# Kernel optimization log

Hardware: AMD Instinct MI355X
Metric: run time of the kernel (lower is better)

## Reference

```python
import jax, jax.numpy as jnp
import numpy as np
import math

B, T, D, H = 4, 1024, 1024, 16
DK = D // H
EPS = 1e-12  # F.normalize eps

def setup_inputs() -> dict:
    key = jax.random.key(0)
    ks = jax.random.split(key, 6)
    xav = math.sqrt(6.0 / (D + D))  # xavier_uniform bound for square Linear
    x = jax.random.normal(ks[0], (B, T, D), dtype=jnp.float32)
    Wq = jax.random.uniform(ks[1], (D, D), jnp.float32, -xav, xav)
    Wk = jax.random.uniform(ks[2], (D, D), jnp.float32, -xav, xav)
    Wv = jax.random.uniform(ks[3], (D, D), jnp.float32, -xav, xav)
    Wo = jax.random.uniform(ks[4], (D, D), jnp.float32, -xav, xav)
    logit_g = math.log(0.9 / 0.1)
    logit_l = math.log(0.1 / 0.9)
    W_gamma = jnp.zeros((H,), jnp.float32)
    b_gamma = jnp.full((H,), logit_g, jnp.float32)
    W_lambda = jnp.zeros((H,), jnp.float32)
    b_lambda = jnp.full((H,), logit_l, jnp.float32)
    return {"x": x, "Wq": Wq, "Wk": Wk, "Wv": Wv, "Wo": Wo,
            "W_gamma": W_gamma, "b_gamma": b_gamma,
            "W_lambda": W_lambda, "b_lambda": b_lambda}

def reference(x, Wq, Wk, Wv, Wo, W_gamma, b_gamma, W_lambda, b_lambda):
    b, t, d = x.shape
    # projections (torch Linear: x @ W.T), split heads -> [T, B, H, dk] for scan
    def proj(W):
        return jnp.einsum('btd,ed->bte', x, W).reshape(b, t, H, DK).transpose(1, 0, 2, 3)
    q = proj(Wq)
    k = proj(Wk)
    v = proj(Wv)
    # L2-normalize k along dk (F.normalize semantics)
    k = k / jnp.maximum(jnp.linalg.norm(k, axis=-1, keepdims=True), EPS)
    k_bar = k.mean(axis=-1)  # [T, B, H]
    gamma = jax.nn.sigmoid(W_gamma * k_bar + b_gamma)
    lam = jax.nn.sigmoid(W_lambda * k_bar + b_lambda)
    rho = (1.0 - lam) * gamma  # [T, B, H]

    S0 = jnp.zeros((b, H, DK, DK), x.dtype)

    def step(S, inp):
        q_t, k_t, v_t, rho_t = inp  # [B,H,dk] x3, [B,H]
        r = rho_t[..., None, None]
        S = r * S + (1.0 - r) * jnp.einsum('bhv,bhk->bhvk', v_t, k_t)
        y_t = jnp.einsum('bhv,bhvk->bhk', q_t, S)
        return S, y_t

    _, ys = jax.lax.scan(step, S0, (q, k, v, rho))  # ys: [T, B, H, dk]
    out = ys.transpose(1, 0, 2, 3).reshape(b, t, d)
    return jnp.einsum('btd,ed->bte', out, Wo)
```

## Files before the change

### kernel.cpp

```cpp
#include <hip/hip_runtime.h>
#include <hip/hip_bf16.h>


typedef __bf16 b16x8 __attribute__((ext_vector_type(8)));
typedef float  f32x4 __attribute__((ext_vector_type(4)));
typedef unsigned short u16x8 __attribute__((ext_vector_type(8)));
using bf16_t = __hip_bfloat16;

#define AS1C(p) ((const __attribute__((address_space(1))) void*)(p))
#define AS3(p)  ((__attribute__((address_space(3))) void*)(p))

__device__ __forceinline__ void g2l16(const void* g, void* l) {
  __builtin_amdgcn_global_load_lds(AS1C(g), AS3(l), 16, 0, 0);
}
__device__ __forceinline__ void g2l4(const void* g, void* l) {
  __builtin_amdgcn_global_load_lds(AS1C(g), AS3(l), 4, 0, 0);
}

__device__ __forceinline__ unsigned short f2b(float x) {
  unsigned u = __float_as_uint(x);
  return (unsigned short)((u + 0x7FFFu + ((u >> 16) & 1u)) >> 16);
}
__device__ __forceinline__ float b2f(unsigned short b) {
  return __uint_as_float(((unsigned)b) << 16);
}

__device__ __forceinline__ int wire_flag(const unsigned* __restrict__ x, int tid) {
  unsigned u = x[tid & 63];
  int e = (int)((u >> 23) & 0xFF);
  unsigned long long m = __ballot(e >= 95 && e <= 135);
  return (__popcll(m) >= 32) ? 1 : 0;
}

__global__ __launch_bounds__(256)
void convert_all(const void* __restrict__ x,
                 const void* __restrict__ w0, const void* __restrict__ w1,
                 const void* __restrict__ w2, const void* __restrict__ w3,
                 unsigned short* __restrict__ xb,
                 unsigned short* __restrict__ wb0, unsigned short* __restrict__ wb1,
                 unsigned short* __restrict__ wb2, unsigned short* __restrict__ wb3)
{
  const int fm = wire_flag((const unsigned*)x, threadIdx.x);
  const long i8 = ((long)blockIdx.x * 256 + threadIdx.x) * 8;
  const void* src; unsigned short* dst; long off;
  if (i8 < 4194304) { src = x; dst = xb; off = i8; }
  else {
    long j = i8 - 4194304;
    int w = (int)(j >> 20); off = j & 1048575;
    src = (w == 0) ? w0 : (w == 1) ? w1 : (w == 2) ? w2 : w3;
    dst = (w == 0) ? wb0 : (w == 1) ? wb1 : (w == 2) ? wb2 : wb3;
  }
  if (fm) {
    const float4 a = *(const float4*)((const float*)src + off);
    const float4 b = *(const float4*)((const float*)src + off + 4);
    u16x8 o;
    o[0] = f2b(a.x); o[1] = f2b(a.y); o[2] = f2b(a.z); o[3] = f2b(a.w);
    o[4] = f2b(b.x); o[5] = f2b(b.y); o[6] = f2b(b.z); o[7] = f2b(b.w);
    *(u16x8*)(dst + off) = o;
  } else {
    *(int4*)(dst + off) = *(const int4*)((const unsigned short*)src + off);
  }
}

__global__ __launch_bounds__(256)
void gemm_qkv(const unsigned* __restrict__ xraw,
              const bf16_t* __restrict__ A,
              const bf16_t* __restrict__ B0, const bf16_t* __restrict__ B1,
              const bf16_t* __restrict__ B2,
              unsigned short* __restrict__ C0, unsigned short* __restrict__ C1,
              unsigned short* __restrict__ C2,
              const void* __restrict__ Wg, const void* __restrict__ bg,
              const void* __restrict__ Wl, const void* __restrict__ bl,
              float* __restrict__ rho)
{
  constexpr int K = 1024, N = 1024;
  const int z = blockIdx.z;
  const bf16_t* B = (z == 0) ? B0 : (z == 1) ? B1 : B2;
  unsigned short* C = (z == 0) ? C0 : (z == 1) ? C1 : C2;
  __shared__ __align__(16) unsigned short As[128 * 32];
  __shared__ __align__(16) unsigned short Bs[128 * 32];
  const int tid  = threadIdx.x;
  const int lane = tid & 63;
  const int wave = tid >> 6;
  const int wm = wave >> 1, wn = wave & 1;
  const int quad = lane >> 4, tm = lane & 15;
  const long row0 = (long)blockIdx.y * 128;
  const long col0 = (long)blockIdx.x * 128;

  f32x4 acc[4][4];
#pragma unroll
  for (int i = 0; i < 4; ++i)
#pragma unroll
    for (int j = 0; j < 4; ++j) acc[i][j] = (f32x4){0.f, 0.f, 0.f, 0.f};

  const int sr = tid >> 2;
  const int scc = tid & 3;
  const int qg = (scc - (sr >> 1)) & 3;
  const bf16_t* ap = A + (row0 + sr) * (long)K + qg * 8;
  const bf16_t* bp = B + (col0 + sr) * (long)K + qg * 8;
  unsigned short* la = As + tid * 8;
  unsigned short* lb = Bs + tid * 8;
  const int cc = (quad + ((tm >> 1) & 3)) & 3;

  for (int kt = 0; kt < K; kt += 32) {
    __syncthreads();
    g2l16(ap + kt,           la);
    g2l16(ap + 64l * K + kt, la + 2048);
    g2l16(bp + kt,           lb);
    g2l16(bp + 64l * K + kt, lb + 2048);
    __syncthreads();

    b16x8 af[4], bfr[4];
#pragma unroll
    for (int i = 0; i < 4; ++i)
      af[i] = *(const b16x8*)&As[(wm * 64 + i * 16 + tm) * 32 + cc * 8];
#pragma unroll
    for (int j = 0; j < 4; ++j)
      bfr[j] = *(const b16x8*)&Bs[(wn * 64 + j * 16 + tm) * 32 + cc * 8];
#pragma unroll
    for (int i = 0; i < 4; ++i)
#pragma unroll
      for (int j = 0; j < 4; ++j)
        acc[i][j] = __builtin_amdgcn_mfma_f32_16x16x32_bf16(af[i], bfr[j], acc[i][j], 0, 0, 0);
  }

  if (z != 1) {
#pragma unroll
    for (int i = 0; i < 4; ++i)
#pragma unroll
      for (int j = 0; j < 4; ++j)
#pragma unroll
        for (int r = 0; r < 4; ++r) {
          long row = row0 + wm * 64 + i * 16 + quad * 4 + r;
          long col = col0 + wn * 64 + j * 16 + tm;
          C[row * N + col] = f2b(acc[i][j][r]);
        }
  } else {
    const int fm = wire_flag(xraw, tid);
    const int h = blockIdx.x * 2 + wn;
    float wgv, bgv, wlv, blv;
    if (fm) {
      wgv = ((const float*)Wg)[h]; bgv = ((const float*)bg)[h];
      wlv = ((const float*)Wl)[h]; blv = ((const float*)bl)[h];
    } else {
      wgv = b2f(((const unsigned short*)Wg)[h]); bgv = b2f(((const unsigned short*)bg)[h]);
      wlv = b2f(((const unsigned short*)Wl)[h]); blv = b2f(((const unsigned short*)bl)[h]);
    }
#pragma unroll
    for (int i = 0; i < 4; ++i)
#pragma unroll
      for (int r = 0; r < 4; ++r) {
        float ss = 0.f, sv = 0.f;
#pragma unroll
        for (int j = 0; j < 4; ++j) {
          const float v = acc[i][j][r];
          ss += v * v; sv += v;
        }
#pragma unroll
        for (int m = 1; m < 16; m <<= 1) {
          ss += __shfl_xor(ss, m);
          sv += __shfl_xor(sv, m);
        }
        const float inv = 1.f / fmaxf(sqrtf(ss), 1e-12f);
        const long row = row0 + wm * 64 + i * 16 + quad * 4 + r;
#pragma unroll
        for (int j = 0; j < 4; ++j)
          C[row * N + col0 + wn * 64 + j * 16 + tm] = f2b(acc[i][j][r] * inv);
        if (tm == 0) {
          const float kbar = sv * inv * (1.f / 64.f);
          const float gm = 1.f / (1.f + expf(-(wgv * kbar + bgv)));
          const float lm = 1.f / (1.f + expf(-(wlv * kbar + blv)));
          const int b = (int)(row >> 10), t = (int)(row & 1023);
          rho[(size_t)(b * 16 + h) * 1024 + t] = (1.f - lm) * gm;
        }
      }
  }
}

__global__ __launch_bounds__(256)
void gemm_out64(const unsigned* __restrict__ xraw,
                const bf16_t* __restrict__ A, const bf16_t* __restrict__ B,
                void* __restrict__ C)
{
  constexpr int K = 1024, N = 1024;
  __shared__ __align__(16) unsigned short As[64 * 64];
  __shared__ __align__(16) unsigned short Bs[64 * 64];
  const int tid  = threadIdx.x;
  const int lane = tid & 63;
  const int wave = tid >> 6;
  const int quad = lane >> 4, tm = lane & 15;
  const long row0 = (long)blockIdx.y * 64;
  const long col0 = (long)blockIdx.x * 64;

  f32x4 acc[4];
#pragma unroll
  for (int i = 0; i < 4; ++i) acc[i] = (f32x4){0.f, 0.f, 0.f, 0.f};

  const int sr = tid >> 2;
  const int scc = tid & 3;
  const int qg = (scc - (sr >> 1)) & 3;
  const bf16_t* ap = A + (row0 + sr) * (long)K + qg * 8;
  const bf16_t* bp = B + (col0 + sr) * (long)K + qg * 8;
  unsigned short* la = As + tid * 8;
  unsigned short* lb = Bs + tid * 8;
  const int cc = (quad + ((tm >> 1) & 3)) & 3;

  for (int kt = 0; kt < K; kt += 64) {
    __syncthreads();
    g2l16(ap + kt,      la);
    g2l16(ap + kt + 32, la + 2048);
    g2l16(bp + kt,      lb);
    g2l16(bp + kt + 32, lb + 2048);
    __syncthreads();

    b16x8 bf0 = *(const b16x8*)&Bs[(wave * 16 + tm) * 32 + cc * 8];
    b16x8 bf1 = *(const b16x8*)&Bs[2048 + (wave * 16 + tm) * 32 + cc * 8];
#pragma unroll
    for (int i = 0; i < 4; ++i) {
      b16x8 a0 = *(const b16x8*)&As[(i * 16 + tm) * 32 + cc * 8];
      b16x8 a1 = *(const b16x8*)&As[2048 + (i * 16 + tm) * 32 + cc * 8];
      acc[i] = __builtin_amdgcn_mfma_f32_16x16x32_bf16(a0, bf0, acc[i], 0, 0, 0);
      acc[i] = __builtin_amdgcn_mfma_f32_16x16x32_bf16(a1, bf1, acc[i], 0, 0, 0);
    }
  }

  const int fm = wire_flag(xraw, tid);
#pragma unroll
  for (int i = 0; i < 4; ++i)
#pragma unroll
    for (int r = 0; r < 4; ++r) {
      const long row = row0 + i * 16 + quad * 4 + r;
      const long col = col0 + wave * 16 + tm;
      const float v = acc[i][r];
      if (fm) ((float*)C)[row * N + col] = v;
      else    ((unsigned short*)C)[row * N + col] = f2b(v);
    }
}

__device__ __forceinline__ void stage_chunk(const unsigned short* G, int n0c, int h,
                                            unsigned short* lds, int tid) {
#pragma unroll
  for (int sh = 0; sh < 2; ++sh) {
    const int idx = sh * 256 + tid;
    const int row = idx >> 3, col = (idx & 7) * 8;
    g2l16(G + (size_t)(n0c + row) * 1024 + h * 64 + col, lds + idx * 8);
  }
}

__device__ __forceinline__ void rho_scan(const float* rho_s, float* aw, float* cw,
                                         int tid) {
  if (tid < 64) {
    const float r = rho_s[tid];
    float p = r;
#pragma unroll
    for (int d = 1; d < 64; d <<= 1) {
      float o = __shfl_up(p, d);
      if (tid >= d) p *= o;
    }
    aw[tid] = p;
    cw[tid] = (1.f - r) / p;
  }
}

__global__ __launch_bounds__(256)
void chunk_outer(const unsigned short* __restrict__ Kb, const unsigned short* __restrict__ Vb,
                 const float* __restrict__ rho, float* __restrict__ Ug,
                 float* __restrict__ A_g)
{
  __shared__ __align__(16) unsigned short ks[4096];
  __shared__ __align__(16) unsigned short vs[4096];
  __shared__ float rho_s[64];
  __shared__ float aw[64], cw[64];
  const int tid = threadIdx.x;
  const int bid = blockIdx.x;
  const int bh = bid >> 4, c = bid & 15;
  const int b = bh >> 4, h = bh & 15;
  const int n0c = b * 1024 + c * 64;
  const int lane = tid & 63, wave = tid >> 6;
  const int quad = lane >> 4, tm = lane & 15;

  stage_chunk(Kb, n0c, h, ks, tid);
  stage_chunk(Vb, n0c, h, vs, tid);
  if (tid < 64) g2l4(rho + (size_t)bh * 1024 + c * 64 + tid, rho_s + tid);
  __syncthreads();
  rho_scan(rho_s, aw, cw, tid);
  __syncthreads();

  const __bf16* ksb = (const __bf16*)ks;
  const __bf16* vsb = (const __bf16*)vs;
  const float Ac = aw[63];
  const int wv = 16 * wave + tm;

#pragma unroll
  for (int j4 = 0; j4 < 4; ++j4) {
    const int kc = 16 * j4 + tm;
    f32x4 acc = (f32x4){0.f, 0.f, 0.f, 0.f};
#pragma unroll
    for (int kk = 0; kk < 2; ++kk) {
      const int kbase = kk * 32 + quad * 8;
      b16x8 af, bf;
#pragma unroll
      for (int j = 0; j < 8; ++j) {
        const int s = kbase + j;
        af[j] = vsb[s * 64 + wv];
        bf[j] = (__bf16)(Ac * cw[s] * (float)ksb[s * 64 + kc]);
      }
      acc = __builtin_amdgcn_mfma_f32_16x16x32_bf16(af, bf, acc, 0, 0, 0);
    }
#pragma unroll
    for (int r = 0; r < 4; ++r) {
      const int v = 16 * wave + quad * 4 + r;
      Ug[(size_t)bid * 4096 + v * 64 + 16 * j4 + tm] = acc[r];
    }
  }
  if (tid == 0) A_g[bid] = Ac;
}

__global__ __launch_bounds__(256)
void chunk_scan(const float* __restrict__ Ug, const float* __restrict__ A_g,
                unsigned short* __restrict__ Sp)
{
  const int bh = blockIdx.x;
  const int off = threadIdx.x * 16;
  float S[16];
#pragma unroll
  for (int i = 0; i < 16; ++i) S[i] = 0.f;

  for (int c = 0; c < 16; ++c) {
    const size_t base = ((size_t)bh * 16 + c) * 4096 + off;
    u16x8 o0, o1;
#pragma unroll
    for (int i = 0; i < 8; ++i) { o0[i] = f2b(S[i]); o1[i] = f2b(S[8 + i]); }
    *(u16x8*)(Sp + base)     = o0;
    *(u16x8*)(Sp + base + 8) = o1;
    const float Ac = A_g[bh * 16 + c];
#pragma unroll
    for (int i4 = 0; i4 < 4; ++i4) {
      const float4 u = *(const float4*)(Ug + base + i4 * 4);
      S[i4 * 4 + 0] = Ac * S[i4 * 4 + 0] + u.x;
      S[i4 * 4 + 1] = Ac * S[i4 * 4 + 1] + u.y;
      S[i4 * 4 + 2] = Ac * S[i4 * 4 + 2] + u.z;
      S[i4 * 4 + 3] = Ac * S[i4 * 4 + 3] + u.w;
    }
  }
}

__global__ __launch_bounds__(256)
void chunk_y(const unsigned short* __restrict__ Qb, const unsigned short* __restrict__ Kb,
             const unsigned short* __restrict__ Vb, const unsigned short* __restrict__ Sp,
             const float* __restrict__ rho, unsigned short* __restrict__ Yb)
{
  __shared__ __align__(16) unsigned short qs[4096];
  __shared__ __align__(16) unsigned short ks[4096];
  __shared__ __align__(16) unsigned short vs[4096];
  __shared__ __align__(16) unsigned short ss[4096];
  __shared__ __align__(16) unsigned short pt[4096];
  __shared__ float rho_s[64];
  __shared__ float aw[64], cw[64];
  const int tid = threadIdx.x;
  const int bid = blockIdx.x;
  const int bh = bid >> 4, c = bid & 15;
  const int b = bh >> 4, h = bh & 15;
  const int n0c = b * 1024 + c * 64;
  const int lane = tid & 63, wave = tid >> 6;
  const int quad = lane >> 4, tm = lane & 15;

  stage_chunk(Qb, n0c, h, qs, tid);
  stage_chunk(Kb, n0c, h, ks, tid);
  stage_chunk(Vb, n0c, h, vs, tid);
#pragma unroll
  for (int sh = 0; sh < 2; ++sh) {
    const int idx = sh * 256 + tid;
    g2l16(Sp + (size_t)bid * 4096 + idx * 8, ss + idx * 8);
  }
  if (tid < 64) g2l4(rho + (size_t)bh * 1024 + c * 64 + tid, rho_s + tid);
  __syncthreads();
  rho_scan(rho_s, aw, cw, tid);
  __syncthreads();

  const __bf16* qsb = (const __bf16*)qs;
  const __bf16* ksb = (const __bf16*)ks;
  const __bf16* vsb = (const __bf16*)vs;
  const __bf16* ssb = (const __bf16*)ss;
  __bf16* ptb = (__bf16*)pt;

  b16x8 af_q[2];
#pragma unroll
  for (int kk = 0; kk < 2; ++kk)
    af_q[kk] = *(const b16x8*)&qsb[(16 * wave + tm) * 64 + kk * 32 + quad * 8];

#pragma unroll
  for (int j4 = 0; j4 < 4; ++j4) {
    f32x4 acc = (f32x4){0.f, 0.f, 0.f, 0.f};
#pragma unroll
    for (int kk = 0; kk < 2; ++kk) {
      const b16x8 bf = *(const b16x8*)&vsb[(16 * j4 + tm) * 64 + kk * 32 + quad * 8];
      acc = __builtin_amdgcn_mfma_f32_16x16x32_bf16(af_q[kk], bf, acc, 0, 0, 0);
    }
    const int s = 16 * j4 + tm;
    const float cws = cw[s];
#pragma unroll
    for (int r = 0; r < 4; ++r) {
      const int t = 16 * wave + quad * 4 + r;
      const float w = (s <= t) ? aw[t] * cws : 0.f;
      ptb[t * 64 + s] = (__bf16)(acc[r] * w);
    }
  }

  const float at = aw[16 * wave + tm];
  b16x8 af_qs[2], af_p[2];
#pragma unroll
  for (int kk = 0; kk < 2; ++kk) {
    b16x8 t8;
#pragma unroll
    for (int j = 0; j < 8; ++j) t8[j] = (__bf16)(at * (float)af_q[kk][j]);
    af_qs[kk] = t8;
    af_p[kk] = *(const b16x8*)&ptb[(16 * wave + tm) * 64 + kk * 32 + quad * 8];
  }

#pragma unroll
  for (int j4 = 0; j4 < 4; ++j4) {
    const int kc = 16 * j4 + tm;
    f32x4 acc = (f32x4){0.f, 0.f, 0.f, 0.f};
#pragma unroll
    for (int kk = 0; kk < 2; ++kk) {
      const int kbase = kk * 32 + quad * 8;
      b16x8 bk, bs;
#pragma unroll
      for (int j = 0; j < 8; ++j) {
        bk[j] = ksb[(kbase + j) * 64 + kc];
        bs[j] = ssb[(kbase + j) * 64 + kc];
      }
      acc = __builtin_amdgcn_mfma_f32_16x16x32_bf16(af_p[kk],  bk, acc, 0, 0, 0);
      acc = __builtin_amdgcn_mfma_f32_16x16x32_bf16(af_qs[kk], bs, acc, 0, 0, 0);
    }
#pragma unroll
    for (int r = 0; r < 4; ++r) {
      const int t = 16 * wave + quad * 4 + r;
      Yb[(size_t)(n0c + t) * 1024 + h * 64 + kc] = f2b(acc[r]);
    }
  }
}

extern "C" void kernel_launch(void* const* d_in, const int* in_sizes, int n_in,
                              void* d_out, int out_size, void* d_ws, size_t ws_size,
                              hipStream_t stream) {
  const void* x  = d_in[0];
  const void* Wq = d_in[1];
  const void* Wk = d_in[2];
  const void* Wv = d_in[3];
  const void* Wo = d_in[4];

  char* ws = (char*)d_ws;
  const size_t MB = 1ull << 20;
  unsigned short* x_b  = (unsigned short*)(ws);
  unsigned short* Wq_b = (unsigned short*)(ws + 8 * MB);
  unsigned short* Wk_b = (unsigned short*)(ws + 10 * MB);
  unsigned short* Wv_b = (unsigned short*)(ws + 12 * MB);
  unsigned short* Wo_b = (unsigned short*)(ws + 14 * MB);
  unsigned short* Qb = (unsigned short*)(ws + 16 * MB);
  unsigned short* Kb = (unsigned short*)(ws + 24 * MB);
  unsigned short* Vb = (unsigned short*)(ws + 32 * MB);
  unsigned short* Yb = (unsigned short*)(ws + 40 * MB);
  float*  Ug   = (float*)(ws + 48 * MB);
  unsigned short* Sp = (unsigned short*)(ws + 64 * MB);
  float*  rh   = (float*)(ws + 72 * MB);
  float*  A_g  = (float*)(ws + 72 * MB + 256 * 1024);

  dim3 blk(256);
  convert_all<<<dim3(4096), blk, 0, stream>>>(x, Wq, Wk, Wv, Wo,
                                              x_b, Wq_b, Wk_b, Wv_b, Wo_b);
  gemm_qkv<<<dim3(8, 32, 3), blk, 0, stream>>>((const unsigned*)x,
      (const bf16_t*)x_b, (const bf16_t*)Wq_b, (const bf16_t*)Wk_b, (const bf16_t*)Wv_b,
      Qb, Kb, Vb, d_in[5], d_in[6], d_in[7], d_in[8], rh);
  chunk_outer<<<dim3(1024), blk, 0, stream>>>(Kb, Vb, rh, Ug, A_g);
  chunk_scan<<<dim3(64), blk, 0, stream>>>(Ug, A_g, Sp);
  chunk_y<<<dim3(1024), blk, 0, stream>>>(Qb, Kb, Vb, Sp, rh, Yb);
  gemm_out64<<<dim3(16, 64), blk, 0, stream>>>((const unsigned*)x,
      (const bf16_t*)Yb, (const bf16_t*)Wo_b, d_out);
}
```

Before: 184.0 us.

## Swizzle LDS tiles, remap GEMM blocks per XCD, bf16 Ug, parallelize chunk scan

Flattens the GEMM grids and remaps block indices so neighbouring tiles share an XCD, aiming for better L2 reuse. Chunk kernels now stage tiles with an XOR swizzle and transpose K/V into padded LDS buffers, so MFMA operands are read as vectors instead of strided scalar gathers. Ug is stored as bf16 instead of fp32, which halves that traffic at some precision cost. The chunk scan is spread across 1024 blocks with one element per thread instead of 64 blocks.

```diff
diff --git a/kernel.cpp b/kernel.cpp
--- a/kernel.cpp
+++ b/kernel.cpp
@@ -74,7 +74,11 @@
               float* __restrict__ rho)
 {
   constexpr int K = 1024, N = 1024;
-  const int z = blockIdx.z;
+  const int flat = blockIdx.x;
+  const int xcd = flat & 7, sl = flat >> 3;
+  const int z = sl >> 5, t5 = sl & 31;
+  const int bx = ((xcd & 1) << 2) | (t5 & 3);
+  const int by = ((xcd >> 1) << 3) | (t5 >> 2);
   const bf16_t* B = (z == 0) ? B0 : (z == 1) ? B1 : B2;
   unsigned short* C = (z == 0) ? C0 : (z == 1) ? C1 : C2;
   __shared__ __align__(16) unsigned short As[128 * 32];
@@ -84,8 +88,8 @@
   const int wave = tid >> 6;
   const int wm = wave >> 1, wn = wave & 1;
   const int quad = lane >> 4, tm = lane & 15;
-  const long row0 = (long)blockIdx.y * 128;
-  const long col0 = (long)blockIdx.x * 128;
+  const long row0 = (long)by * 128;
+  const long col0 = (long)bx * 128;
 
   f32x4 acc[4][4];
 #pragma unroll
@@ -137,7 +141,7 @@
         }
   } else {
     const int fm = wire_flag(xraw, tid);
-    const int h = blockIdx.x * 2 + wn;
+    const int h = bx * 2 + wn;
     float wgv, bgv, wlv, blv;
     if (fm) {
       wgv = ((const float*)Wg)[h]; bgv = ((const float*)bg)[h];
@@ -183,14 +187,18 @@
                 void* __restrict__ C)
 {
   constexpr int K = 1024, N = 1024;
+  const int flat = blockIdx.x;
+  const int xcd = flat & 7, sl = flat >> 3;
+  const int bx = sl & 15;
+  const int by = (xcd << 3) | (sl >> 4);
   __shared__ __align__(16) unsigned short As[64 * 64];
   __shared__ __align__(16) unsigned short Bs[64 * 64];
   const int tid  = threadIdx.x;
   const int lane = tid & 63;
   const int wave = tid >> 6;
   const int quad = lane >> 4, tm = lane & 15;
-  const long row0 = (long)blockIdx.y * 64;
-  const long col0 = (long)blockIdx.x * 64;
+  const long row0 = (long)by * 64;
+  const long col0 = (long)bx * 64;
 
   f32x4 acc[4];
 #pragma unroll
@@ -237,18 +245,53 @@
     }
 }
 
-__device__ __forceinline__ void stage_chunk(const unsigned short* G, int n0c, int h,
-                                            unsigned short* lds, int tid) {
+__device__ __forceinline__ void stage_chunk_x(const unsigned short* G, int n0c, int h,
+                                              unsigned short* lds, int tid) {
 #pragma unroll
   for (int sh = 0; sh < 2; ++sh) {
     const int idx = sh * 256 + tid;
-    const int row = idx >> 3, col = (idx & 7) * 8;
-    g2l16(G + (size_t)(n0c + row) * 1024 + h * 64 + col, lds + idx * 8);
-  }
+    const int row = idx >> 3, c2 = idx & 7;
+    const int gc = c2 ^ (row & 7);
+    g2l16(G + (size_t)(n0c + row) * 1024 + h * 64 + gc * 8, lds + idx * 8);
+  }
+}
+__device__ __forceinline__ void stage_blk_x(const unsigned short* G,
+                                            unsigned short* lds, int tid) {
+#pragma unroll
+  for (int sh = 0; sh < 2; ++sh) {
+    const int idx = sh * 256 + tid;
+    const int row = idx >> 3, c2 = idx & 7;
+    const int gc = c2 ^ (row & 7);
+    g2l16(G + row * 64 + gc * 8, lds + idx * 8);
+  }
+}
+__device__ __forceinline__ b16x8 rdx(const unsigned short* lds, int row, int k0) {
+  return *(const b16x8*)&lds[row * 64 + (((k0 >> 3) ^ (row & 7)) << 3)];
+}
+__device__ __forceinline__ float rdx1(const unsigned short* lds, int row, int col) {
+  return b2f(lds[row * 64 + (((col >> 3) ^ (row & 7)) << 3) + (col & 7)]);
+}
+
+__device__ __forceinline__ void transpose_x(const unsigned short* src,
+                                            unsigned short* dst,
+                                            const float* sc, int tid) {
+  const int kc = tid & 63;
+  const int s4 = (tid >> 6) * 16;
+  u16x8 o0, o1;
+#pragma unroll
+  for (int i = 0; i < 16; ++i) {
+    const int s = s4 + i;
+    float v = rdx1(src, s, kc);
+    if (sc) v *= sc[s];
+    const unsigned short b = f2b(v);
+    if (i < 8) o0[i] = b; else o1[i - 8] = b;
+  }
+  *(u16x8*)&dst[kc * 72 + s4]     = o0;
+  *(u16x8*)&dst[kc * 72 + s4 + 8] = o1;
 }
 
 __device__ __forceinline__ void rho_scan(const float* rho_s, float* aw, float* cw,
-                                         int tid) {
+                                         float* sc, int tid) {
   if (tid < 64) {
     const float r = rho_s[tid];
     float p = r;
@@ -258,19 +301,23 @@
       if (tid >= d) p *= o;
     }
     aw[tid] = p;
-    cw[tid] = (1.f - r) / p;
+    const float c = (1.f - r) / p;
+    cw[tid] = c;
+    const float Ac = __shfl(p, 63);
+    sc[tid] = Ac * c;
   }
 }
 
 __global__ __launch_bounds__(256)
 void chunk_outer(const unsigned short* __restrict__ Kb, const unsigned short* __restrict__ Vb,
-                 const float* __restrict__ rho, float* __restrict__ Ug,
+                 const float* __restrict__ rho, unsigned short* __restrict__ Ug,
                  float* __restrict__ A_g)
 {
   __shared__ __align__(16) unsigned short ks[4096];
   __shared__ __align__(16) unsigned short vs[4096];
-  __shared__ float rho_s[64];
-  __shared__ float aw[64], cw[64];
+  __shared__ __align__(16) unsigned short kt[64 * 72];
+  __shared__ __align__(16) unsigned short vt[64 * 72];
+  __shared__ float rho_s[64], aw[64], cw[64], sc[64];
   const int tid = threadIdx.x;
   const int bid = blockIdx.x;
   const int bh = bid >> 4, c = bid & 15;
@@ -279,69 +326,48 @@
   const int lane = tid & 63, wave = tid >> 6;
   const int quad = lane >> 4, tm = lane & 15;
 
-  stage_chunk(Kb, n0c, h, ks, tid);
-  stage_chunk(Vb, n0c, h, vs, tid);
+  stage_chunk_x(Kb, n0c, h, ks, tid);
+  stage_chunk_x(Vb, n0c, h, vs, tid);
   if (tid < 64) g2l4(rho + (size_t)bh * 1024 + c * 64 + tid, rho_s + tid);
   __syncthreads();
-  rho_scan(rho_s, aw, cw, tid);
-  __syncthreads();
-
-  const __bf16* ksb = (const __bf16*)ks;
-  const __bf16* vsb = (const __bf16*)vs;
-  const float Ac = aw[63];
-  const int wv = 16 * wave + tm;
-
+  rho_scan(rho_s, aw, cw, sc, tid);
+  __syncthreads();
+  transpose_x(ks, kt, sc, tid);
+  transpose_x(vs, vt, nullptr, tid);
+  __syncthreads();
+
+  const int mrow = 16 * wave + tm;
+  b16x8 a0 = *(const b16x8*)&kt[mrow * 72 + quad * 8];
+  b16x8 a1 = *(const b16x8*)&kt[mrow * 72 + 32 + quad * 8];
 #pragma unroll
   for (int j4 = 0; j4 < 4; ++j4) {
-    const int kc = 16 * j4 + tm;
+    const int nrow = 16 * j4 + tm;
+    b16x8 b0 = *(const b16x8*)&vt[nrow * 72 + quad * 8];
+    b16x8 b1 = *(const b16x8*)&vt[nrow * 72 + 32 + quad * 8];
     f32x4 acc = (f32x4){0.f, 0.f, 0.f, 0.f};
-#pragma unroll
-    for (int kk = 0; kk < 2; ++kk) {
-      const int kbase = kk * 32 + quad * 8;
-      b16x8 af, bf;
-#pragma unroll
-      for (int j = 0; j < 8; ++j) {
-        const int s = kbase + j;
-        af[j] = vsb[s * 64 + wv];
-        bf[j] = (__bf16)(Ac * cw[s] * (float)ksb[s * 64 + kc]);
-      }
-      acc = __builtin_amdgcn_mfma_f32_16x16x32_bf16(af, bf, acc, 0, 0, 0);
-    }
+    acc = __builtin_amdgcn_mfma_f32_16x16x32_bf16(a0, b0, acc, 0, 0, 0);
+    acc = __builtin_amdgcn_mfma_f32_16x16x32_bf16(a1, b1, acc, 0, 0, 0);
 #pragma unroll
     for (int r = 0; r < 4; ++r) {
-      const int v = 16 * wave + quad * 4 + r;
-      Ug[(size_t)bid * 4096 + v * 64 + 16 * j4 + tm] = acc[r];
-    }
-  }
-  if (tid == 0) A_g[bid] = Ac;
-}
-
-__global__ __launch_bounds__(256)
-void chunk_scan(const float* __restrict__ Ug, const float* __restrict__ A_g,
+      const int kc = 16 * wave + quad * 4 + r;
+      Ug[(size_t)bid * 4096 + kc * 64 + 16 * j4 + tm] = f2b(acc[r]);
+    }
+  }
+  if (tid == 0) A_g[bid] = aw[63];
+}
+
+__global__ __launch_bounds__(256)
+void chunk_scan(const unsigned short* __restrict__ Ug, const float* __restrict__ A_g,
                 unsigned short* __restrict__ Sp)
 {
-  const int bh = blockIdx.x;
-  const int off = threadIdx.x * 16;
-  float S[16];
-#pragma unroll
-  for (int i = 0; i < 16; ++i) S[i] = 0.f;
-
+  const int bh = blockIdx.x >> 4;
+  const int e  = (blockIdx.x & 15) * 256 + threadIdx.x;
+  const size_t base = (size_t)bh * 16 * 4096 + e;
+  float S = 0.f;
+#pragma unroll
   for (int c = 0; c < 16; ++c) {
-    const size_t base = ((size_t)bh * 16 + c) * 4096 + off;
-    u16x8 o0, o1;
-#pragma unroll
-    for (int i = 0; i < 8; ++i) { o0[i] = f2b(S[i]); o1[i] = f2b(S[8 + i]); }
-    *(u16x8*)(Sp + base)     = o0;
-    *(u16x8*)(Sp + base + 8) = o1;
-    const float Ac = A_g[bh * 16 + c];
-#pragma unroll
-    for (int i4 = 0; i4 < 4; ++i4) {
-      const float4 u = *(const float4*)(Ug + base + i4 * 4);
-      S[i4 * 4 + 0] = Ac * S[i4 * 4 + 0] + u.x;
-      S[i4 * 4 + 1] = Ac * S[i4 * 4 + 1] + u.y;
-      S[i4 * 4 + 2] = Ac * S[i4 * 4 + 2] + u.z;
-      S[i4 * 4 + 3] = Ac * S[i4 * 4 + 3] + u.w;
-    }
+    Sp[base + (size_t)c * 4096] = f2b(S);
+    S = A_g[bh * 16 + c] * S + b2f(Ug[base + (size_t)c * 4096]);
   }
 }
 
@@ -354,9 +380,9 @@
   __shared__ __align__(16) unsigned short ks[4096];
   __shared__ __align__(16) unsigned short vs[4096];
   __shared__ __align__(16) unsigned short ss[4096];
-  __shared__ __align__(16) unsigned short pt[4096];
-  __shared__ float rho_s[64];
-  __shared__ float aw[64], cw[64];
+  __shared__ __align__(16) unsigned short kt[64 * 72];
+  __shared__ __align__(16) unsigned short pt[64 * 72];
+  __shared__ float rho_s[64], aw[64], cw[64], sc[64];
   const int tid = threadIdx.x;
   const int bid = blockIdx.x;
   const int bh = bid >> 4, c = bid & 15;
@@ -365,36 +391,29 @@
   const int lane = tid & 63, wave = tid >> 6;
   const int quad = lane >> 4, tm = lane & 15;
 
-  stage_chunk(Qb, n0c, h, qs, tid);
-  stage_chunk(Kb, n0c, h, ks, tid);
-  stage_chunk(Vb, n0c, h, vs, tid);
-#pragma unroll
-  for (int sh = 0; sh < 2; ++sh) {
-    const int idx = sh * 256 + tid;
-    g2l16(Sp + (size_t)bid * 4096 + idx * 8, ss + idx * 8);
-  }
+  stage_chunk_x(Qb, n0c, h, qs, tid);
+  stage_chunk_x(Kb, n0c, h, ks, tid);
+  stage_chunk_x(Vb, n0c, h, vs, tid);
+  stage_blk_x(Sp + (size_t)bid * 4096, ss, tid);
   if (tid < 64) g2l4(rho + (size_t)bh * 1024 + c * 64 + tid, rho_s + tid);
   __syncthreads();
-  rho_scan(rho_s, aw, cw, tid);
-  __syncthreads();
-
-  const __bf16* qsb = (const __bf16*)qs;
-  const __bf16* ksb = (const __bf16*)ks;
-  const __bf16* vsb = (const __bf16*)vs;
-  const __bf16* ssb = (const __bf16*)ss;
+  rho_scan(rho_s, aw, cw, sc, tid);
+  __syncthreads();
+  transpose_x(ks, kt, nullptr, tid);
+
   __bf16* ptb = (__bf16*)pt;
+  const int trow = 16 * wave + tm;
 
   b16x8 af_q[2];
 #pragma unroll
   for (int kk = 0; kk < 2; ++kk)
-    af_q[kk] = *(const b16x8*)&qsb[(16 * wave + tm) * 64 + kk * 32 + quad * 8];
-
+    af_q[kk] = rdx(qs, trow, kk * 32 + quad * 8);
 #pragma unroll
   for (int j4 = 0; j4 < 4; ++j4) {
     f32x4 acc = (f32x4){0.f, 0.f, 0.f, 0.f};
 #pragma unroll
     for (int kk = 0; kk < 2; ++kk) {
-      const b16x8 bf = *(const b16x8*)&vsb[(16 * j4 + tm) * 64 + kk * 32 + quad * 8];
+      const b16x8 bf = rdx(vs, 16 * j4 + tm, kk * 32 + quad * 8);
       acc = __builtin_amdgcn_mfma_f32_16x16x32_bf16(af_q[kk], bf, acc, 0, 0, 0);
     }
     const int s = 16 * j4 + tm;
@@ -403,11 +422,11 @@
     for (int r = 0; r < 4; ++r) {
       const int t = 16 * wave + quad * 4 + r;
       const float w = (s <= t) ? aw[t] * cws : 0.f;
-      ptb[t * 64 + s] = (__bf16)(acc[r] * w);
-    }
-  }
-
-  const float at = aw[16 * wave + tm];
+      ptb[t * 72 + s] = (__bf16)(acc[r] * w);
+    }
+  }
+
+  const float at = aw[trow];
   b16x8 af_qs[2], af_p[2];
 #pragma unroll
   for (int kk = 0; kk < 2; ++kk) {
@@ -415,8 +434,9 @@
 #pragma unroll
     for (int j = 0; j < 8; ++j) t8[j] = (__bf16)(at * (float)af_q[kk][j]);
     af_qs[kk] = t8;
-    af_p[kk] = *(const b16x8*)&ptb[(16 * wave + tm) * 64 + kk * 32 + quad * 8];
-  }
+    af_p[kk] = *(const b16x8*)&pt[trow * 72 + kk * 32 + quad * 8];
+  }
+  __syncthreads();
 
 #pragma unroll
   for (int j4 = 0; j4 < 4; ++j4) {
@@ -425,12 +445,8 @@
 #pragma unroll
     for (int kk = 0; kk < 2; ++kk) {
       const int kbase = kk * 32 + quad * 8;
-      b16x8 bk, bs;
-#pragma unroll
-      for (int j = 0; j < 8; ++j) {
-        bk[j] = ksb[(kbase + j) * 64 + kc];
-        bs[j] = ssb[(kbase + j) * 64 + kc];
-      }
+      const b16x8 bk = *(const b16x8*)&kt[kc * 72 + kbase];
+      const b16x8 bs = rdx(ss, kc, kbase);
       acc = __builtin_amdgcn_mfma_f32_16x16x32_bf16(af_p[kk],  bk, acc, 0, 0, 0);
       acc = __builtin_amdgcn_mfma_f32_16x16x32_bf16(af_qs[kk], bs, acc, 0, 0, 0);
     }
@@ -462,7 +478,7 @@
   unsigned short* Kb = (unsigned short*)(ws + 24 * MB);
   unsigned short* Vb = (unsigned short*)(ws + 32 * MB);
   unsigned short* Yb = (unsigned short*)(ws + 40 * MB);
-  float*  Ug   = (float*)(ws + 48 * MB);
+  unsigned short* Ug = (unsigned short*)(ws + 48 * MB);
   unsigned short* Sp = (unsigned short*)(ws + 64 * MB);
   float*  rh   = (float*)(ws + 72 * MB);
   float*  A_g  = (float*)(ws + 72 * MB + 256 * 1024);
@@ -470,12 +486,12 @@
   dim3 blk(256);
   convert_all<<<dim3(4096), blk, 0, stream>>>(x, Wq, Wk, Wv, Wo,
                                               x_b, Wq_b, Wk_b, Wv_b, Wo_b);
-  gemm_qkv<<<dim3(8, 32, 3), blk, 0, stream>>>((const unsigned*)x,
+  gemm_qkv<<<dim3(768), blk, 0, stream>>>((const unsigned*)x,
       (const bf16_t*)x_b, (const bf16_t*)Wq_b, (const bf16_t*)Wk_b, (const bf16_t*)Wv_b,
       Qb, Kb, Vb, d_in[5], d_in[6], d_in[7], d_in[8], rh);
   chunk_outer<<<dim3(1024), blk, 0, stream>>>(Kb, Vb, rh, Ug, A_g);
-  chunk_scan<<<dim3(64), blk, 0, stream>>>(Ug, A_g, Sp);
+  chunk_scan<<<dim3(1024), blk, 0, stream>>>(Ug, A_g, Sp);
   chunk_y<<<dim3(1024), blk, 0, stream>>>(Qb, Kb, Vb, Sp, rh, Yb);
-  gemm_out64<<<dim3(16, 64), blk, 0, stream>>>((const unsigned*)x,
+  gemm_out64<<<dim3(1024), blk, 0, stream>>>((const unsigned*)x,
       (const bf16_t*)Yb, (const bf16_t*)Wo_b, d_out);
 }
```

Measured after the change: 168.9 us. 8.2% less time.
